# Optimization experiments

Hardware: AMD Instinct MI355X
Metric: run time of the kernel (lower is better)

Reference implementation:

```python
import jax, jax.numpy as jnp
import numpy as np

N_ATOMS = 50000
N_PAIRS = 600000
F = 128          # number_of_per_atom_features
RBF = 16         # number_of_radial_basis_functions
N_INT_RES = 3    # interaction residual blocks
N_OUT_RES = 2    # output residual blocks
N_PROPS = 2      # atomic properties (hardcoded in PhysNetModule)


def setup_inputs() -> dict:
    key = jax.random.key(0)
    ks = jax.random.split(key, 24)
    s = 1.0 / np.sqrt(F)
    inp = {
        "atomic_embedding": jax.random.normal(ks[0], (N_ATOMS, F), jnp.float32),
        "f_ij": jax.random.uniform(ks[1], (N_PAIRS, RBF), jnp.float32),
        "pair_indices": jax.random.randint(ks[2], (2, N_PAIRS), 0, N_ATOMS, jnp.int64),
        # attention_mask: Dense(RBF -> F, bias=False); zero-init in source, randomized here
        "Wg": jax.random.normal(ks[3], (RBF, F), jnp.float32) * (1.0 / np.sqrt(RBF)),
        "Wi": jax.random.normal(ks[4], (F, F), jnp.float32) * s,
        "bi": jnp.zeros((F,), jnp.float32),
        "Wj": jax.random.normal(ks[5], (F, F), jnp.float32) * s,
        "bj": jnp.zeros((F,), jnp.float32),
        "Wv": jax.random.normal(ks[6], (F, F), jnp.float32) * s,
        "bv": jnp.zeros((F,), jnp.float32),
        "gate": jnp.ones((F,), jnp.float32),
        "int_res_W1": jax.random.normal(ks[7], (N_INT_RES, F, F), jnp.float32) * s,
        "int_res_b1": jnp.zeros((N_INT_RES, F), jnp.float32),
        "int_res_W2": jax.random.normal(ks[8], (N_INT_RES, F, F), jnp.float32) * s,
        "int_res_b2": jnp.zeros((N_INT_RES, F), jnp.float32),
        "out_res_W1": jax.random.normal(ks[9], (N_OUT_RES, F, F), jnp.float32) * s,
        "out_res_b1": jnp.zeros((N_OUT_RES, F), jnp.float32),
        "out_res_W2": jax.random.normal(ks[10], (N_OUT_RES, F, F), jnp.float32) * s,
        "out_res_b2": jnp.zeros((N_OUT_RES, F), jnp.float32),
        # output head: Dense(F -> 2), zero-init in source, randomized here
        "Wo": jax.random.normal(ks[11], (F, N_PROPS), jnp.float32) * s,
        "bo": jnp.zeros((N_PROPS,), jnp.float32),
    }
    return inp


def _residual(x, W1, b1, W2, b2):
    # PhysNetResidual: x + Dense(Dense(act(x), act), linear)
    h = jax.nn.softplus(x)
    h = jax.nn.softplus(h @ W1 + b1)
    return x + h @ W2 + b2


def reference(atomic_embedding, f_ij, pair_indices,
              Wg, Wi, bi, Wj, bj, Wv, bv, gate,
              int_res_W1, int_res_b1, int_res_W2, int_res_b2,
              out_res_W1, out_res_b1, out_res_W2, out_res_b2,
              Wo, bo):
    idx_i, idx_j = pair_indices[0], pair_indices[1]

    # --- interaction module ---
    e = jax.nn.softplus(atomic_embedding)            # [N, F]
    g = f_ij @ Wg                                    # [E, F] attention mask (no bias)
    u = jax.nn.softplus(e @ Wi + bi)                 # [N, F] interaction_i
    m_j = jax.nn.softplus(e[idx_j] @ Wj + bj) * g    # [E, F] gather + gate
    u = u.at[idx_i].add(m_j)                         # scatter_add to i-atoms
    for k in range(N_INT_RES):
        u = _residual(u, int_res_W1[k], int_res_b1[k], int_res_W2[k], int_res_b2[k])
    u = jax.nn.softplus(u)
    v = gate * e + (u @ Wv + bv)                     # updated embedding [N, F]

    # --- output module ---
    x = v
    for k in range(N_OUT_RES):
        x = _residual(x, out_res_W1[k], out_res_b1[k], out_res_W2[k], out_res_b2[k])
    prediction = x @ Wo + bo                         # [N, 2]
    return prediction, v
```

## Files before the change

### kernel.cpp

```cpp
#include <hip/hip_runtime.h>
#include <math.h>

#define F 128
#define RBF 16
#define NATOMS 50000
#define NPAIRS 600000
#define NBLK 196

typedef float f32x4 __attribute__((ext_vector_type(4)));
typedef short s16x8 __attribute__((ext_vector_type(8)));

__device__ __forceinline__ float sp(float x) {
    return fmaxf(x, 0.f) + __logf(1.f + __expf(-fabsf(x)));
}
__device__ __forceinline__ short f2bf(float x) {
    unsigned u = __float_as_uint(x);
    u += 0x7FFFu + ((u >> 16) & 1u);
    return (short)(u >> 16);
}
__device__ __forceinline__ float bf2f(unsigned short u) {
    return __uint_as_float(((unsigned)u) << 16);
}

__global__ __launch_bounds__(256) void prep_w_k(
    const float* __restrict__ Wi, const float* __restrict__ Wj, const float* __restrict__ Wv,
    const float* __restrict__ iW1, const float* __restrict__ iW2,
    const float* __restrict__ oW1, const float* __restrict__ oW2,
    short* __restrict__ wpack)
{
    int o = blockIdx.x * 256 + threadIdx.x;
    if (o >= 13 * 16384) return;
    int mat = o >> 14;
    int rem = o & 16383;
    int j = rem & 7;
    int lane = (rem >> 3) & 63;
    int nt = (rem >> 9) & 7;
    int kc = rem >> 12;
    int k = kc * 32 + ((lane >> 4) << 3) + j;
    int n = nt * 16 + (lane & 15);
    const float* src;
    if (mat == 0) src = Wi;
    else if (mat == 1) src = Wj;
    else if (mat == 2) src = Wv;
    else if (mat < 6) src = iW1 + (size_t)(mat - 3) * 16384;
    else if (mat < 9) src = iW2 + (size_t)(mat - 6) * 16384;
    else if (mat < 11) src = oW1 + (size_t)(mat - 9) * 16384;
    else src = oW2 + (size_t)(mat - 11) * 16384;
    wpack[o] = f2bf(src[(size_t)k * F + n]);
}

template <int PRE>
__device__ __forceinline__ s16x8 load_a_frag(const float* __restrict__ in,
                                             int row, int nrows, int kc, int cg)
{
    s16x8 a;
    if (row < nrows) {
        const float* p = in + (size_t)row * F + kc * 32 + cg * 8;
        float4 x0 = *(const float4*)p;
        float4 x1 = *(const float4*)(p + 4);
        if (PRE) {
            x0.x = sp(x0.x); x0.y = sp(x0.y); x0.z = sp(x0.z); x0.w = sp(x0.w);
            x1.x = sp(x1.x); x1.y = sp(x1.y); x1.z = sp(x1.z); x1.w = sp(x1.w);
        }
        a[0] = f2bf(x0.x); a[1] = f2bf(x0.y); a[2] = f2bf(x0.z); a[3] = f2bf(x0.w);
        a[4] = f2bf(x1.x); a[5] = f2bf(x1.y); a[6] = f2bf(x1.z); a[7] = f2bf(x1.w);
    } else {
#pragma unroll
        for (int i = 0; i < 8; ++i) a[i] = 0;
    }
    return a;
}

template <int PRE, int POST, int DUAL>
__global__ __launch_bounds__(256) void mgemm_k(
    const float* __restrict__ in, const short* __restrict__ wpA,
    const float* __restrict__ bA, float* __restrict__ outA,
    const short* __restrict__ wpB, const float* __restrict__ bB,
    unsigned short* __restrict__ outB, int nrows)
{
    const int lane = threadIdx.x & 63;
    const int wv = threadIdx.x >> 6;
    const int grp = wv >> 1, half = wv & 1;
    const int r0 = blockIdx.x * 32 + grp * 16;
    const int cl = lane & 15, cg = lane >> 4;
    const int ntb = half * 4;

    s16x8 afr[4];
#pragma unroll
    for (int kc = 0; kc < 4; ++kc) afr[kc] = load_a_frag<PRE>(in, r0 + cl, nrows, kc, cg);

    f32x4 accA[4], accB[4];
#pragma unroll
    for (int n = 0; n < 4; ++n) {
        accA[n] = (f32x4){0.f, 0.f, 0.f, 0.f};
        accB[n] = (f32x4){0.f, 0.f, 0.f, 0.f};
    }

#pragma unroll
    for (int kc = 0; kc < 4; ++kc) {
        const s16x8* bpA = (const s16x8*)wpA + (size_t)(kc * 8 + ntb) * 64 + lane;
#pragma unroll
        for (int n = 0; n < 4; ++n) {
            s16x8 b = bpA[n * 64];
            accA[n] = __builtin_amdgcn_mfma_f32_16x16x32_bf16(afr[kc], b, accA[n], 0, 0, 0);
        }
        if (DUAL) {
            const s16x8* bpB = (const s16x8*)wpB + (size_t)(kc * 8 + ntb) * 64 + lane;
#pragma unroll
            for (int n = 0; n < 4; ++n) {
                s16x8 b = bpB[n * 64];
                accB[n] = __builtin_amdgcn_mfma_f32_16x16x32_bf16(afr[kc], b, accB[n], 0, 0, 0);
            }
        }
    }

#pragma unroll
    for (int n = 0; n < 4; ++n) {
        const int col = (ntb + n) * 16 + cl;
        const float ba = bA[col];
        const float bb = DUAL ? bB[col] : 0.f;
#pragma unroll
        for (int q = 0; q < 4; ++q) {
            const int row = r0 + cg * 4 + q;
            if (row < nrows) {
                const size_t o = (size_t)row * F + col;
                float val = accA[n][q] + ba;
                if (POST == 1) val = sp(val);
                outA[o] = val;
                if (DUAL) outB[o] = (unsigned short)f2bf(sp(accB[n][q] + bb));
            }
        }
    }
}

__device__ __forceinline__ void gemm_half(const short* __restrict__ wp, int lane, int ntb,
                                          const s16x8 afr[4], f32x4 acc[4])
{
#pragma unroll
    for (int n = 0; n < 4; ++n) acc[n] = (f32x4){0.f, 0.f, 0.f, 0.f};
#pragma unroll
    for (int kc = 0; kc < 4; ++kc) {
        const s16x8* bp = (const s16x8*)wp + (size_t)(kc * 8 + ntb) * 64 + lane;
#pragma unroll
        for (int n = 0; n < 4; ++n) {
            s16x8 b = bp[n * 64];
            acc[n] = __builtin_amdgcn_mfma_f32_16x16x32_bf16(afr[kc], b, acc[n], 0, 0, 0);
        }
    }
}

template <int FIRST>
__device__ __forceinline__ void residual_half(
    const float* __restrict__ u, f32x4 xreg[4],
    unsigned short* __restrict__ S, unsigned short* __restrict__ H,
    const short* __restrict__ wp1, const float* __restrict__ b1,
    const short* __restrict__ wp2, const float* __restrict__ b2,
    int r0, int nrows, int lane, int cl, int cg, int ntb)
{
    s16x8 afr[4];
    if (FIRST) {
#pragma unroll
        for (int kc = 0; kc < 4; ++kc) afr[kc] = load_a_frag<1>(u, r0 + cl, nrows, kc, cg);
    } else {
#pragma unroll
        for (int kc = 0; kc < 4; ++kc)
            afr[kc] = *(const s16x8*)(S + cl * 144 + kc * 32 + cg * 8);
    }
    f32x4 acc[4];
    gemm_half(wp1, lane, ntb, afr, acc);
#pragma unroll
    for (int n = 0; n < 4; ++n) {
        const int col = (ntb + n) * 16 + cl;
        const float bb = b1[col];
#pragma unroll
        for (int q = 0; q < 4; ++q)
            H[(cg * 4 + q) * 144 + col] = (unsigned short)f2bf(sp(acc[n][q] + bb));
    }
    __syncthreads();
#pragma unroll
    for (int kc = 0; kc < 4; ++kc)
        afr[kc] = *(const s16x8*)(H + cl * 144 + kc * 32 + cg * 8);
    gemm_half(wp2, lane, ntb, afr, acc);
#pragma unroll
    for (int n = 0; n < 4; ++n) {
        const int col = (ntb + n) * 16 + cl;
        const float bb = b2[col];
#pragma unroll
        for (int q = 0; q < 4; ++q) {
            float xv = xreg[n][q] + acc[n][q] + bb;
            xreg[n][q] = xv;
            S[(cg * 4 + q) * 144 + col] = (unsigned short)f2bf(sp(xv));
        }
    }
    __syncthreads();
}

__global__ __launch_bounds__(256, 4) void fused_tail_k(
    const float* __restrict__ u, const float* __restrict__ emb,
    const float* __restrict__ gate,
    const short* __restrict__ wpI1, const float* __restrict__ ib1,
    const short* __restrict__ wpI2, const float* __restrict__ ib2,
    const short* __restrict__ wpWv, const float* __restrict__ bvv,
    const short* __restrict__ wpO1, const float* __restrict__ ob1,
    const short* __restrict__ wpO2, const float* __restrict__ ob2,
    const float* __restrict__ Wo, const float* __restrict__ bo,
    float* __restrict__ vout, float* __restrict__ pred, int nrows)
{
    __shared__ unsigned short Sb[2][16 * 144];
    __shared__ unsigned short Hb[2][16 * 144];
    const int lane = threadIdx.x & 63;
    const int wv = threadIdx.x >> 6;
    const int grp = wv >> 1, half = wv & 1;
    const int r0 = blockIdx.x * 32 + grp * 16;
    const int cl = lane & 15, cg = lane >> 4;
    const int ntb = half * 4;
    unsigned short* S = Sb[grp];
    unsigned short* H = Hb[grp];

    f32x4 xreg[4];
#pragma unroll
    for (int n = 0; n < 4; ++n) {
        const int col = (ntb + n) * 16 + cl;
#pragma unroll
        for (int q = 0; q < 4; ++q) {
            const int row = r0 + cg * 4 + q;
            xreg[n][q] = (row < nrows) ? u[(size_t)row * F + col] : 0.f;
        }
    }

    residual_half<1>(u, xreg, S, H, wpI1, ib1, wpI2, ib2,
                     r0, nrows, lane, cl, cg, ntb);
    for (int k = 1; k < 3; ++k)
        residual_half<0>(u, xreg, S, H,
                         wpI1 + (size_t)k * 16384, ib1 + (size_t)k * F,
                         wpI2 + (size_t)k * 16384, ib2 + (size_t)k * F,
                         r0, nrows, lane, cl, cg, ntb);

    {
        s16x8 afr[4];
#pragma unroll
        for (int kc = 0; kc < 4; ++kc)
            afr[kc] = *(const s16x8*)(S + cl * 144 + kc * 32 + cg * 8);
        f32x4 acc[4];
        gemm_half(wpWv, lane, ntb, afr, acc);
        __syncthreads();
#pragma unroll
        for (int n = 0; n < 4; ++n) {
            const int col = (ntb + n) * 16 + cl;
            const float bb = bvv[col];
            const float gt = gate[col];
#pragma unroll
            for (int q = 0; q < 4; ++q) {
                const int row = r0 + cg * 4 + q;
                float val = acc[n][q] + bb;
                if (row < nrows) {
                    const size_t o = (size_t)row * F + col;
                    val += gt * sp(emb[o]);
                    vout[o] = val;
                }
                xreg[n][q] = val;
                S[(cg * 4 + q) * 144 + col] = (unsigned short)f2bf(sp(val));
            }
        }
        __syncthreads();
    }

    for (int k = 0; k < 2; ++k)
        residual_half<0>(u, xreg, S, H,
                         wpO1 + (size_t)k * 16384, ob1 + (size_t)k * F,
                         wpO2 + (size_t)k * 16384, ob2 + (size_t)k * F,
                         r0, nrows, lane, cl, cg, ntb);

    {
        float2 wo[4];
#pragma unroll
        for (int n = 0; n < 4; ++n)
            wo[n] = *(const float2*)(Wo + (size_t)((ntb + n) * 16 + cl) * 2);
        float* sc = (float*)S;
#pragma unroll
        for (int q = 0; q < 4; ++q) {
            float a0 = xreg[0][q] * wo[0].x + xreg[1][q] * wo[1].x
                     + xreg[2][q] * wo[2].x + xreg[3][q] * wo[3].x;
            float a1 = xreg[0][q] * wo[0].y + xreg[1][q] * wo[1].y
                     + xreg[2][q] * wo[2].y + xreg[3][q] * wo[3].y;
#pragma unroll
            for (int m = 1; m < 16; m <<= 1) {
                a0 += __shfl_xor(a0, m);
                a1 += __shfl_xor(a1, m);
            }
            if (cl == 0) {
                sc[half * 32 + (cg * 4 + q) * 2 + 0] = a0;
                sc[half * 32 + (cg * 4 + q) * 2 + 1] = a1;
            }
        }
        __syncthreads();
        if (half == 0 && lane < 16) {
            const int row = r0 + lane;
            if (row < nrows) {
                pred[(size_t)row * 2 + 0] = sc[lane * 2 + 0] + sc[32 + lane * 2 + 0] + bo[0];
                pred[(size_t)row * 2 + 1] = sc[lane * 2 + 1] + sc[32 + lane * 2 + 1] + bo[1];
            }
        }
    }
}

__global__ void zero_k(int* __restrict__ p, int n)
{
    int i = blockIdx.x * blockDim.x + threadIdx.x;
    if (i < n) p[i] = 0;
}

__global__ void hist_k(const int* __restrict__ idx_i, int* __restrict__ counts)
{
    int p = blockIdx.x * blockDim.x + threadIdx.x;
    if (p < NPAIRS) atomicAdd(&counts[idx_i[p]], 1);
}

__global__ __launch_bounds__(256) void scan1_k(
    const int* __restrict__ counts, int* __restrict__ bsum)
{
    __shared__ int red[256];
    const int t = threadIdx.x;
    const int i = blockIdx.x * 256 + t;
    red[t] = (i < NATOMS) ? counts[i] : 0;
    __syncthreads();
#pragma unroll
    for (int s = 128; s > 0; s >>= 1) {
        if (t < s) red[t] += red[t + s];
        __syncthreads();
    }
    if (t == 0) bsum[blockIdx.x] = red[0];
}

__global__ __launch_bounds__(256) void scan2_k(
    const int* __restrict__ bsum, int* __restrict__ bbase, int* __restrict__ offsets)
{
    __shared__ int sh[256];
    const int t = threadIdx.x;
    const int v = (t < NBLK) ? bsum[t] : 0;
    sh[t] = v;
    __syncthreads();
#pragma unroll
    for (int s = 1; s < 256; s <<= 1) {
        int add = (t >= s) ? sh[t - s] : 0;
        __syncthreads();
        sh[t] += add;
        __syncthreads();
    }
    if (t < NBLK) bbase[t] = sh[t] - v;
    if (t == 0) offsets[NATOMS] = NPAIRS;
}

__global__ __launch_bounds__(256) void scan3_k(
    const int* __restrict__ counts, const int* __restrict__ bbase,
    int* __restrict__ offsets, int* __restrict__ cursor)
{
    __shared__ int sh[256];
    const int t = threadIdx.x;
    const int i = blockIdx.x * 256 + t;
    const int v = (i < NATOMS) ? counts[i] : 0;
    sh[t] = v;
    __syncthreads();
#pragma unroll
    for (int s = 1; s < 256; s <<= 1) {
        int add = (t >= s) ? sh[t - s] : 0;
        __syncthreads();
        sh[t] += add;
        __syncthreads();
    }
    if (i < NATOMS) {
        const int off = bbase[blockIdx.x] + sh[t] - v;
        offsets[i] = off;
        cursor[i] = off;
    }
}

__global__ void scatter_k(const int* __restrict__ idx_i, const int* __restrict__ idx_j,
                          int* __restrict__ cursor, int* __restrict__ plist,
                          int* __restrict__ jlist)
{
    int p = blockIdx.x * blockDim.x + threadIdx.x;
    if (p < NPAIRS) {
        int pos = atomicAdd(&cursor[idx_i[p]], 1);
        plist[pos] = p;
        jlist[pos] = idx_j[p];
    }
}

__device__ __forceinline__ void gpair(const float* __restrict__ fp,
                                      const float* wg0, const float* wg1,
                                      float& g0, float& g1)
{
    float4 A = ((const float4*)fp)[0], B = ((const float4*)fp)[1];
    float4 C = ((const float4*)fp)[2], D = ((const float4*)fp)[3];
    g0 = A.x*wg0[0] + A.y*wg0[1] + A.z*wg0[2] + A.w*wg0[3]
       + B.x*wg0[4] + B.y*wg0[5] + B.z*wg0[6] + B.w*wg0[7]
       + C.x*wg0[8] + C.y*wg0[9] + C.z*wg0[10] + C.w*wg0[11]
       + D.x*wg0[12] + D.y*wg0[13] + D.z*wg0[14] + D.w*wg0[15];
    g1 = A.x*wg1[0] + A.y*wg1[1] + A.z*wg1[2] + A.w*wg1[3]
       + B.x*wg1[4] + B.y*wg1[5] + B.z*wg1[6] + B.w*wg1[7]
       + C.x*wg1[8] + C.y*wg1[9] + C.z*wg1[10] + C.w*wg1[11]
       + D.x*wg1[12] + D.y*wg1[13] + D.z*wg1[14] + D.w*wg1[15];
}

__global__ __launch_bounds__(256) void gather_k(
    const unsigned short* __restrict__ mj, const float* __restrict__ fij,
    const int* __restrict__ jlist, const int* __restrict__ plist,
    const int* __restrict__ offsets, const float* __restrict__ Wg,
    float* __restrict__ u)
{
    const int lane = threadIdx.x & 63;
    const int atom = blockIdx.x * 4 + (threadIdx.x >> 6);
    const int f0 = lane * 2;

    float wg0[16], wg1[16];
#pragma unroll
    for (int r = 0; r < 16; ++r) {
        float2 w = *(const float2*)(Wg + r * F + f0);
        wg0[r] = w.x; wg1[r] = w.y;
    }

    const int k0 = offsets[atom], k1 = offsets[atom + 1];
    float acc0 = 0.f, acc1 = 0.f;

    for (int k = k0; k < k1; k += 8) {
        int jv[8], pv[8];
#pragma unroll
        for (int t = 0; t < 8; ++t) {
            const int kk = (k + t < k1) ? (k + t) : (k1 - 1);
            jv[t] = jlist[kk];
            pv[t] = plist[kk];
        }
        unsigned m[8];
        const float* fp[8];
#pragma unroll
        for (int t = 0; t < 8; ++t) {
            const int js = __builtin_amdgcn_readfirstlane(jv[t]);
            const int ps = __builtin_amdgcn_readfirstlane(pv[t]);
            m[t] = *(const unsigned*)(mj + (size_t)js * F + f0);
            fp[t] = fij + (size_t)ps * RBF;
        }
#pragma unroll
        for (int t = 0; t < 8; ++t) {
            float g0, g1;
            gpair(fp[t], wg0, wg1, g0, g1);
            if (k + t >= k1) { g0 = 0.f; g1 = 0.f; }
            acc0 += bf2f((unsigned short)(m[t] & 0xFFFF)) * g0;
            acc1 += bf2f((unsigned short)(m[t] >> 16))    * g1;
        }
    }

    float2* up = (float2*)(u + (size_t)atom * F + f0);
    float2 old = *up;
    old.x += acc0; old.y += acc1;
    *up = old;
}

extern "C" void kernel_launch(void* const* d_in, const int* in_sizes, int n_in,
                              void* d_out, int out_size, void* d_ws, size_t ws_size,
                              hipStream_t stream)
{
    const float* emb   = (const float*)d_in[0];
    const float* fij   = (const float*)d_in[1];
    const int*   pidx  = (const int*)d_in[2];
    const float* Wg    = (const float*)d_in[3];
    const float* Wi    = (const float*)d_in[4];
    const float* bi    = (const float*)d_in[5];
    const float* Wj    = (const float*)d_in[6];
    const float* bj    = (const float*)d_in[7];
    const float* Wv    = (const float*)d_in[8];
    const float* bv    = (const float*)d_in[9];
    const float* gate  = (const float*)d_in[10];
    const float* iW1   = (const float*)d_in[11];
    const float* ib1   = (const float*)d_in[12];
    const float* iW2   = (const float*)d_in[13];
    const float* ib2   = (const float*)d_in[14];
    const float* oW1   = (const float*)d_in[15];
    const float* ob1   = (const float*)d_in[16];
    const float* oW2   = (const float*)d_in[17];
    const float* ob2   = (const float*)d_in[18];
    const float* Wo    = (const float*)d_in[19];
    const float* bo    = (const float*)d_in[20];

    const int* idx_i = pidx;
    const int* idx_j = pidx + NPAIRS;

    float* outp = (float*)d_out;
    float* pred = outp;
    float* v    = outp + (size_t)NATOMS * 2;

    const size_t NF = (size_t)NATOMS * F;
    float* u = (float*)d_ws;
    unsigned short* mj = (unsigned short*)(u + NF);
    short* wpack = (short*)(mj + NF);
    int* counts   = (int*)(wpack + 13 * 16384);
    int* offsets  = counts + NATOMS;
    int* cursor   = offsets + NATOMS + 1;
    int* plist    = cursor + NATOMS;
    int* jlist    = plist + NPAIRS;
    int* bsum     = jlist + NPAIRS;
    int* bbase    = bsum + NBLK;

    const short* wpWi = wpack;
    const short* wpWj = wpack + 1 * 16384;
    const short* wpWv = wpack + 2 * 16384;
    const short* wpI1 = wpack + 3 * 16384;
    const short* wpI2 = wpack + 6 * 16384;
    const short* wpO1 = wpack + 9 * 16384;
    const short* wpO2 = wpack + 11 * 16384;

    prep_w_k<<<(13 * 16384 + 255) / 256, 256, 0, stream>>>(Wi, Wj, Wv, iW1, iW2, oW1, oW2, wpack);
    zero_k<<<(NATOMS + 255) / 256, 256, 0, stream>>>(counts, NATOMS);
    hist_k<<<(NPAIRS + 255) / 256, 256, 0, stream>>>(idx_i, counts);
    scan1_k<<<NBLK, 256, 0, stream>>>(counts, bsum);
    scan2_k<<<1, 256, 0, stream>>>(bsum, bbase, offsets);
    scan3_k<<<NBLK, 256, 0, stream>>>(counts, bbase, offsets, cursor);
    scatter_k<<<(NPAIRS + 255) / 256, 256, 0, stream>>>(idx_i, idx_j, cursor, plist, jlist);

    mgemm_k<1, 1, 1><<<(NATOMS + 31) / 32, 256, 0, stream>>>(
        emb, wpWi, bi, u, wpWj, bj, mj, NATOMS);

    gather_k<<<(NATOMS + 3) / 4, 256, 0, stream>>>(
        mj, fij, jlist, plist, offsets, Wg, u);

    fused_tail_k<<<(NATOMS + 31) / 32, 256, 0, stream>>>(
        u, emb, gate,
        wpI1, ib1, wpI2, ib2,
        wpWv, bv,
        wpO1, ob1, wpO2, ob2,
        Wo, bo, v, pred, NATOMS);
}
```

Before: 267.6 us.

## Split fused tail across four waves per 16-row tile with swizzled LDS

After: 280.3 us. 4.8% more time.

```diff
diff --git a/kernel.cpp b/kernel.cpp
--- a/kernel.cpp
+++ b/kernel.cpp
@@ -13,13 +13,16 @@
 __device__ __forceinline__ float sp(float x) {
     return fmaxf(x, 0.f) + __logf(1.f + __expf(-fabsf(x)));
 }
-__device__ __forceinline__ short f2bf(float x) {
+__device__ __forceinline__ unsigned short f2bf(float x) {
     unsigned u = __float_as_uint(x);
     u += 0x7FFFu + ((u >> 16) & 1u);
-    return (short)(u >> 16);
+    return (unsigned short)(u >> 16);
 }
 __device__ __forceinline__ float bf2f(unsigned short u) {
     return __uint_as_float(((unsigned)u) << 16);
+}
+__device__ __forceinline__ int lds_idx(int row, int col) {
+    return (row * 144 + col) ^ ((row & 7) << 3);
 }
 
 __global__ __launch_bounds__(256) void prep_w_k(
@@ -46,7 +49,7 @@
     else if (mat < 9) src = iW2 + (size_t)(mat - 6) * 16384;
     else if (mat < 11) src = oW1 + (size_t)(mat - 9) * 16384;
     else src = oW2 + (size_t)(mat - 11) * 16384;
-    wpack[o] = f2bf(src[(size_t)k * F + n]);
+    wpack[o] = (short)f2bf(src[(size_t)k * F + n]);
 }
 
 template <int PRE>
@@ -127,22 +130,22 @@
                 float val = accA[n][q] + ba;
                 if (POST == 1) val = sp(val);
                 outA[o] = val;
-                if (DUAL) outB[o] = (unsigned short)f2bf(sp(accB[n][q] + bb));
+                if (DUAL) outB[o] = f2bf(sp(accB[n][q] + bb));
             }
         }
     }
 }
 
-__device__ __forceinline__ void gemm_half(const short* __restrict__ wp, int lane, int ntb,
-                                          const s16x8 afr[4], f32x4 acc[4])
-{
-#pragma unroll
-    for (int n = 0; n < 4; ++n) acc[n] = (f32x4){0.f, 0.f, 0.f, 0.f};
+__device__ __forceinline__ void gemm_q(const short* __restrict__ wp, int lane, int ntb,
+                                       const s16x8 afr[4], f32x4 acc[2])
+{
+#pragma unroll
+    for (int n = 0; n < 2; ++n) acc[n] = (f32x4){0.f, 0.f, 0.f, 0.f};
 #pragma unroll
     for (int kc = 0; kc < 4; ++kc) {
         const s16x8* bp = (const s16x8*)wp + (size_t)(kc * 8 + ntb) * 64 + lane;
 #pragma unroll
-        for (int n = 0; n < 4; ++n) {
+        for (int n = 0; n < 2; ++n) {
             s16x8 b = bp[n * 64];
             acc[n] = __builtin_amdgcn_mfma_f32_16x16x32_bf16(afr[kc], b, acc[n], 0, 0, 0);
         }
@@ -150,8 +153,8 @@
 }
 
 template <int FIRST>
-__device__ __forceinline__ void residual_half(
-    const float* __restrict__ u, f32x4 xreg[4],
+__device__ __forceinline__ void residual_q(
+    const float* __restrict__ u, f32x4 xreg[2],
     unsigned short* __restrict__ S, unsigned short* __restrict__ H,
     const short* __restrict__ wp1, const float* __restrict__ b1,
     const short* __restrict__ wp2, const float* __restrict__ b2,
@@ -164,38 +167,38 @@
     } else {
 #pragma unroll
         for (int kc = 0; kc < 4; ++kc)
-            afr[kc] = *(const s16x8*)(S + cl * 144 + kc * 32 + cg * 8);
-    }
-    f32x4 acc[4];
-    gemm_half(wp1, lane, ntb, afr, acc);
-#pragma unroll
-    for (int n = 0; n < 4; ++n) {
+            afr[kc] = *(const s16x8*)(S + lds_idx(cl, kc * 32 + cg * 8));
+    }
+    f32x4 acc[2];
+    gemm_q(wp1, lane, ntb, afr, acc);
+#pragma unroll
+    for (int n = 0; n < 2; ++n) {
         const int col = (ntb + n) * 16 + cl;
         const float bb = b1[col];
 #pragma unroll
         for (int q = 0; q < 4; ++q)
-            H[(cg * 4 + q) * 144 + col] = (unsigned short)f2bf(sp(acc[n][q] + bb));
+            H[lds_idx(cg * 4 + q, col)] = f2bf(sp(acc[n][q] + bb));
     }
     __syncthreads();
 #pragma unroll
     for (int kc = 0; kc < 4; ++kc)
-        afr[kc] = *(const s16x8*)(H + cl * 144 + kc * 32 + cg * 8);
-    gemm_half(wp2, lane, ntb, afr, acc);
-#pragma unroll
-    for (int n = 0; n < 4; ++n) {
+        afr[kc] = *(const s16x8*)(H + lds_idx(cl, kc * 32 + cg * 8));
+    gemm_q(wp2, lane, ntb, afr, acc);
+#pragma unroll
+    for (int n = 0; n < 2; ++n) {
         const int col = (ntb + n) * 16 + cl;
         const float bb = b2[col];
 #pragma unroll
         for (int q = 0; q < 4; ++q) {
             float xv = xreg[n][q] + acc[n][q] + bb;
             xreg[n][q] = xv;
-            S[(cg * 4 + q) * 144 + col] = (unsigned short)f2bf(sp(xv));
+            S[lds_idx(cg * 4 + q, col)] = f2bf(sp(xv));
         }
     }
     __syncthreads();
 }
 
-__global__ __launch_bounds__(256, 4) void fused_tail_k(
+__global__ __launch_bounds__(256, 6) void fused_tail_k(
     const float* __restrict__ u, const float* __restrict__ emb,
     const float* __restrict__ gate,
     const short* __restrict__ wpI1, const float* __restrict__ ib1,
@@ -206,20 +209,17 @@
     const float* __restrict__ Wo, const float* __restrict__ bo,
     float* __restrict__ vout, float* __restrict__ pred, int nrows)
 {
-    __shared__ unsigned short Sb[2][16 * 144];
-    __shared__ unsigned short Hb[2][16 * 144];
+    __shared__ unsigned short S[16 * 144];
+    __shared__ unsigned short H[16 * 144];
     const int lane = threadIdx.x & 63;
     const int wv = threadIdx.x >> 6;
-    const int grp = wv >> 1, half = wv & 1;
-    const int r0 = blockIdx.x * 32 + grp * 16;
+    const int r0 = blockIdx.x * 16;
     const int cl = lane & 15, cg = lane >> 4;
-    const int ntb = half * 4;
-    unsigned short* S = Sb[grp];
-    unsigned short* H = Hb[grp];
-
-    f32x4 xreg[4];
-#pragma unroll
-    for (int n = 0; n < 4; ++n) {
+    const int ntb = wv * 2;
+
+    f32x4 xreg[2];
+#pragma unroll
+    for (int n = 0; n < 2; ++n) {
         const int col = (ntb + n) * 16 + cl;
 #pragma unroll
         for (int q = 0; q < 4; ++q) {
@@ -228,24 +228,24 @@
         }
     }
 
-    residual_half<1>(u, xreg, S, H, wpI1, ib1, wpI2, ib2,
-                     r0, nrows, lane, cl, cg, ntb);
+    residual_q<1>(u, xreg, S, H, wpI1, ib1, wpI2, ib2,
+                  r0, nrows, lane, cl, cg, ntb);
     for (int k = 1; k < 3; ++k)
-        residual_half<0>(u, xreg, S, H,
-                         wpI1 + (size_t)k * 16384, ib1 + (size_t)k * F,
-                         wpI2 + (size_t)k * 16384, ib2 + (size_t)k * F,
-                         r0, nrows, lane, cl, cg, ntb);
+        residual_q<0>(u, xreg, S, H,
+                      wpI1 + (size_t)k * 16384, ib1 + (size_t)k * F,
+                      wpI2 + (size_t)k * 16384, ib2 + (size_t)k * F,
+                      r0, nrows, lane, cl, cg, ntb);
 
     {
         s16x8 afr[4];
 #pragma unroll
         for (int kc = 0; kc < 4; ++kc)
-            afr[kc] = *(const s16x8*)(S + cl * 144 + kc * 32 + cg * 8);
-        f32x4 acc[4];
-        gemm_half(wpWv, lane, ntb, afr, acc);
-        __syncthreads();
-#pragma unroll
-        for (int n = 0; n < 4; ++n) {
+            afr[kc] = *(const s16x8*)(S + lds_idx(cl, kc * 32 + cg * 8));
+        f32x4 acc[2];
+        gemm_q(wpWv, lane, ntb, afr, acc);
+        __syncthreads();
+#pragma unroll
+        for (int n = 0; n < 2; ++n) {
             const int col = (ntb + n) * 16 + cl;
             const float bb = bvv[col];
             const float gt = gate[col];
@@ -259,55 +259,49 @@
                     vout[o] = val;
                 }
                 xreg[n][q] = val;
-                S[(cg * 4 + q) * 144 + col] = (unsigned short)f2bf(sp(val));
+                S[lds_idx(cg * 4 + q, col)] = f2bf(sp(val));
             }
         }
         __syncthreads();
     }
 
     for (int k = 0; k < 2; ++k)
-        residual_half<0>(u, xreg, S, H,
-                         wpO1 + (size_t)k * 16384, ob1 + (size_t)k * F,
-                         wpO2 + (size_t)k * 16384, ob2 + (size_t)k * F,
-                         r0, nrows, lane, cl, cg, ntb);
+        residual_q<0>(u, xreg, S, H,
+                      wpO1 + (size_t)k * 16384, ob1 + (size_t)k * F,
+                      wpO2 + (size_t)k * 16384, ob2 + (size_t)k * F,
+                      r0, nrows, lane, cl, cg, ntb);
 
     {
-        float2 wo[4];
-#pragma unroll
-        for (int n = 0; n < 4; ++n)
+        float2 wo[2];
+#pragma unroll
+        for (int n = 0; n < 2; ++n)
             wo[n] = *(const float2*)(Wo + (size_t)((ntb + n) * 16 + cl) * 2);
         float* sc = (float*)S;
 #pragma unroll
         for (int q = 0; q < 4; ++q) {
-            float a0 = xreg[0][q] * wo[0].x + xreg[1][q] * wo[1].x
-                     + xreg[2][q] * wo[2].x + xreg[3][q] * wo[3].x;
-            float a1 = xreg[0][q] * wo[0].y + xreg[1][q] * wo[1].y
-                     + xreg[2][q] * wo[2].y + xreg[3][q] * wo[3].y;
+            float a0 = xreg[0][q] * wo[0].x + xreg[1][q] * wo[1].x;
+            float a1 = xreg[0][q] * wo[0].y + xreg[1][q] * wo[1].y;
 #pragma unroll
             for (int m = 1; m < 16; m <<= 1) {
                 a0 += __shfl_xor(a0, m);
                 a1 += __shfl_xor(a1, m);
             }
             if (cl == 0) {
-                sc[half * 32 + (cg * 4 + q) * 2 + 0] = a0;
-                sc[half * 32 + (cg * 4 + q) * 2 + 1] = a1;
+                sc[wv * 32 + (cg * 4 + q) * 2 + 0] = a0;
+                sc[wv * 32 + (cg * 4 + q) * 2 + 1] = a1;
             }
         }
         __syncthreads();
-        if (half == 0 && lane < 16) {
+        if (wv == 0 && lane < 16) {
             const int row = r0 + lane;
             if (row < nrows) {
-                pred[(size_t)row * 2 + 0] = sc[lane * 2 + 0] + sc[32 + lane * 2 + 0] + bo[0];
-                pred[(size_t)row * 2 + 1] = sc[lane * 2 + 1] + sc[32 + lane * 2 + 1] + bo[1];
+                pred[(size_t)row * 2 + 0] = sc[lane * 2 + 0] + sc[32 + lane * 2 + 0]
+                                          + sc[64 + lane * 2 + 0] + sc[96 + lane * 2 + 0] + bo[0];
+                pred[(size_t)row * 2 + 1] = sc[lane * 2 + 1] + sc[32 + lane * 2 + 1]
+                                          + sc[64 + lane * 2 + 1] + sc[96 + lane * 2 + 1] + bo[1];
             }
         }
     }
-}
-
-__global__ void zero_k(int* __restrict__ p, int n)
-{
-    int i = blockIdx.x * blockDim.x + threadIdx.x;
-    if (i < n) p[i] = 0;
 }
 
 __global__ void hist_k(const int* __restrict__ idx_i, int* __restrict__ counts)
@@ -510,7 +504,7 @@
     const short* wpO2 = wpack + 11 * 16384;
 
     prep_w_k<<<(13 * 16384 + 255) / 256, 256, 0, stream>>>(Wi, Wj, Wv, iW1, iW2, oW1, oW2, wpack);
-    zero_k<<<(NATOMS + 255) / 256, 256, 0, stream>>>(counts, NATOMS);
+    hipMemsetAsync(counts, 0, NATOMS * sizeof(int), stream);
     hist_k<<<(NPAIRS + 255) / 256, 256, 0, stream>>>(idx_i, counts);
     scan1_k<<<NBLK, 256, 0, stream>>>(counts, bsum);
     scan2_k<<<1, 256, 0, stream>>>(bsum, bbase, offsets);
@@ -523,7 +517,7 @@
     gather_k<<<(NATOMS + 3) / 4, 256, 0, stream>>>(
         mj, fij, jlist, plist, offsets, Wg, u);
 
-    fused_tail_k<<<(NATOMS + 31) / 32, 256, 0, stream>>>(
+    fused_tail_k<<<(NATOMS + 15) / 16, 256, 0, stream>>>(
         u, emb, gate,
         wpI1, ib1, wpI2, ib2,
         wpWv, bv,
```

## Fuse gather-scatter aggregation into the residual tail kernel via shared memory

Applied to the files above, without the earlier changes.

New measurement: 306.9 us. +14.7%, slower.

```diff
diff --git a/kernel.cpp b/kernel.cpp
--- a/kernel.cpp
+++ b/kernel.cpp
@@ -13,10 +13,10 @@
 __device__ __forceinline__ float sp(float x) {
     return fmaxf(x, 0.f) + __logf(1.f + __expf(-fabsf(x)));
 }
-__device__ __forceinline__ short f2bf(float x) {
+__device__ __forceinline__ unsigned short f2bf(float x) {
     unsigned u = __float_as_uint(x);
     u += 0x7FFFu + ((u >> 16) & 1u);
-    return (short)(u >> 16);
+    return (unsigned short)(u >> 16);
 }
 __device__ __forceinline__ float bf2f(unsigned short u) {
     return __uint_as_float(((unsigned)u) << 16);
@@ -46,7 +46,7 @@
     else if (mat < 9) src = iW2 + (size_t)(mat - 6) * 16384;
     else if (mat < 11) src = oW1 + (size_t)(mat - 9) * 16384;
     else src = oW2 + (size_t)(mat - 11) * 16384;
-    wpack[o] = f2bf(src[(size_t)k * F + n]);
+    wpack[o] = (short)f2bf(src[(size_t)k * F + n]);
 }
 
 template <int PRE>
@@ -127,7 +127,7 @@
                 float val = accA[n][q] + ba;
                 if (POST == 1) val = sp(val);
                 outA[o] = val;
-                if (DUAL) outB[o] = (unsigned short)f2bf(sp(accB[n][q] + bb));
+                if (DUAL) outB[o] = f2bf(sp(accB[n][q] + bb));
             }
         }
     }
@@ -151,7 +151,7 @@
 
 template <int FIRST>
 __device__ __forceinline__ void residual_half(
-    const float* __restrict__ u, f32x4 xreg[4],
+    const float* __restrict__ u, const float* __restrict__ sug, f32x4 xreg[4],
     unsigned short* __restrict__ S, unsigned short* __restrict__ H,
     const short* __restrict__ wp1, const float* __restrict__ b1,
     const short* __restrict__ wp2, const float* __restrict__ b2,
@@ -159,8 +159,27 @@
 {
     s16x8 afr[4];
     if (FIRST) {
-#pragma unroll
-        for (int kc = 0; kc < 4; ++kc) afr[kc] = load_a_frag<1>(u, r0 + cl, nrows, kc, cg);
+        const int row = r0 + cl;
+#pragma unroll
+        for (int kc = 0; kc < 4; ++kc) {
+            s16x8 a;
+            if (row < nrows) {
+                const float* p = u + (size_t)row * F + kc * 32 + cg * 8;
+                float4 x0 = *(const float4*)p;
+                float4 x1 = *(const float4*)(p + 4);
+                const float* sq = sug + cl * 132 + kc * 32 + cg * 8;
+                f32x4 s0 = *(const f32x4*)sq;
+                f32x4 s1 = *(const f32x4*)(sq + 4);
+                a[0] = f2bf(sp(x0.x + s0.x)); a[1] = f2bf(sp(x0.y + s0.y));
+                a[2] = f2bf(sp(x0.z + s0.z)); a[3] = f2bf(sp(x0.w + s0.w));
+                a[4] = f2bf(sp(x1.x + s1.x)); a[5] = f2bf(sp(x1.y + s1.y));
+                a[6] = f2bf(sp(x1.z + s1.z)); a[7] = f2bf(sp(x1.w + s1.w));
+            } else {
+#pragma unroll
+                for (int i = 0; i < 8; ++i) a[i] = 0;
+            }
+            afr[kc] = a;
+        }
     } else {
 #pragma unroll
         for (int kc = 0; kc < 4; ++kc)
@@ -174,7 +193,7 @@
         const float bb = b1[col];
 #pragma unroll
         for (int q = 0; q < 4; ++q)
-            H[(cg * 4 + q) * 144 + col] = (unsigned short)f2bf(sp(acc[n][q] + bb));
+            H[(cg * 4 + q) * 144 + col] = f2bf(sp(acc[n][q] + bb));
     }
     __syncthreads();
 #pragma unroll
@@ -189,202 +208,10 @@
         for (int q = 0; q < 4; ++q) {
             float xv = xreg[n][q] + acc[n][q] + bb;
             xreg[n][q] = xv;
-            S[(cg * 4 + q) * 144 + col] = (unsigned short)f2bf(sp(xv));
+            S[(cg * 4 + q) * 144 + col] = f2bf(sp(xv));
         }
     }
     __syncthreads();
-}
-
-__global__ __launch_bounds__(256, 4) void fused_tail_k(
-    const float* __restrict__ u, const float* __restrict__ emb,
-    const float* __restrict__ gate,
-    const short* __restrict__ wpI1, const float* __restrict__ ib1,
-    const short* __restrict__ wpI2, const float* __restrict__ ib2,
-    const short* __restrict__ wpWv, const float* __restrict__ bvv,
-    const short* __restrict__ wpO1, const float* __restrict__ ob1,
-    const short* __restrict__ wpO2, const float* __restrict__ ob2,
-    const float* __restrict__ Wo, const float* __restrict__ bo,
-    float* __restrict__ vout, float* __restrict__ pred, int nrows)
-{
-    __shared__ unsigned short Sb[2][16 * 144];
-    __shared__ unsigned short Hb[2][16 * 144];
-    const int lane = threadIdx.x & 63;
-    const int wv = threadIdx.x >> 6;
-    const int grp = wv >> 1, half = wv & 1;
-    const int r0 = blockIdx.x * 32 + grp * 16;
-    const int cl = lane & 15, cg = lane >> 4;
-    const int ntb = half * 4;
-    unsigned short* S = Sb[grp];
-    unsigned short* H = Hb[grp];
-
-    f32x4 xreg[4];
-#pragma unroll
-    for (int n = 0; n < 4; ++n) {
-        const int col = (ntb + n) * 16 + cl;
-#pragma unroll
-        for (int q = 0; q < 4; ++q) {
-            const int row = r0 + cg * 4 + q;
-            xreg[n][q] = (row < nrows) ? u[(size_t)row * F + col] : 0.f;
-        }
-    }
-
-    residual_half<1>(u, xreg, S, H, wpI1, ib1, wpI2, ib2,
-                     r0, nrows, lane, cl, cg, ntb);
-    for (int k = 1; k < 3; ++k)
-        residual_half<0>(u, xreg, S, H,
-                         wpI1 + (size_t)k * 16384, ib1 + (size_t)k * F,
-                         wpI2 + (size_t)k * 16384, ib2 + (size_t)k * F,
-                         r0, nrows, lane, cl, cg, ntb);
-
-    {
-        s16x8 afr[4];
-#pragma unroll
-        for (int kc = 0; kc < 4; ++kc)
-            afr[kc] = *(const s16x8*)(S + cl * 144 + kc * 32 + cg * 8);
-        f32x4 acc[4];
-        gemm_half(wpWv, lane, ntb, afr, acc);
-        __syncthreads();
-#pragma unroll
-        for (int n = 0; n < 4; ++n) {
-            const int col = (ntb + n) * 16 + cl;
-            const float bb = bvv[col];
-            const float gt = gate[col];
-#pragma unroll
-            for (int q = 0; q < 4; ++q) {
-                const int row = r0 + cg * 4 + q;
-                float val = acc[n][q] + bb;
-                if (row < nrows) {
-                    const size_t o = (size_t)row * F + col;
-                    val += gt * sp(emb[o]);
-                    vout[o] = val;
-                }
-                xreg[n][q] = val;
-                S[(cg * 4 + q) * 144 + col] = (unsigned short)f2bf(sp(val));
-            }
-        }
-        __syncthreads();
-    }
-
-    for (int k = 0; k < 2; ++k)
-        residual_half<0>(u, xreg, S, H,
-                         wpO1 + (size_t)k * 16384, ob1 + (size_t)k * F,
-                         wpO2 + (size_t)k * 16384, ob2 + (size_t)k * F,
-                         r0, nrows, lane, cl, cg, ntb);
-
-    {
-        float2 wo[4];
-#pragma unroll
-        for (int n = 0; n < 4; ++n)
-            wo[n] = *(const float2*)(Wo + (size_t)((ntb + n) * 16 + cl) * 2);
-        float* sc = (float*)S;
-#pragma unroll
-        for (int q = 0; q < 4; ++q) {
-            float a0 = xreg[0][q] * wo[0].x + xreg[1][q] * wo[1].x
-                     + xreg[2][q] * wo[2].x + xreg[3][q] * wo[3].x;
-            float a1 = xreg[0][q] * wo[0].y + xreg[1][q] * wo[1].y
-                     + xreg[2][q] * wo[2].y + xreg[3][q] * wo[3].y;
-#pragma unroll
-            for (int m = 1; m < 16; m <<= 1) {
-                a0 += __shfl_xor(a0, m);
-                a1 += __shfl_xor(a1, m);
-            }
-            if (cl == 0) {
-                sc[half * 32 + (cg * 4 + q) * 2 + 0] = a0;
-                sc[half * 32 + (cg * 4 + q) * 2 + 1] = a1;
-            }
-        }
-        __syncthreads();
-        if (half == 0 && lane < 16) {
-            const int row = r0 + lane;
-            if (row < nrows) {
-                pred[(size_t)row * 2 + 0] = sc[lane * 2 + 0] + sc[32 + lane * 2 + 0] + bo[0];
-                pred[(size_t)row * 2 + 1] = sc[lane * 2 + 1] + sc[32 + lane * 2 + 1] + bo[1];
-            }
-        }
-    }
-}
-
-__global__ void zero_k(int* __restrict__ p, int n)
-{
-    int i = blockIdx.x * blockDim.x + threadIdx.x;
-    if (i < n) p[i] = 0;
-}
-
-__global__ void hist_k(const int* __restrict__ idx_i, int* __restrict__ counts)
-{
-    int p = blockIdx.x * blockDim.x + threadIdx.x;
-    if (p < NPAIRS) atomicAdd(&counts[idx_i[p]], 1);
-}
-
-__global__ __launch_bounds__(256) void scan1_k(
-    const int* __restrict__ counts, int* __restrict__ bsum)
-{
-    __shared__ int red[256];
-    const int t = threadIdx.x;
-    const int i = blockIdx.x * 256 + t;
-    red[t] = (i < NATOMS) ? counts[i] : 0;
-    __syncthreads();
-#pragma unroll
-    for (int s = 128; s > 0; s >>= 1) {
-        if (t < s) red[t] += red[t + s];
-        __syncthreads();
-    }
-    if (t == 0) bsum[blockIdx.x] = red[0];
-}
-
-__global__ __launch_bounds__(256) void scan2_k(
-    const int* __restrict__ bsum, int* __restrict__ bbase, int* __restrict__ offsets)
-{
-    __shared__ int sh[256];
-    const int t = threadIdx.x;
-    const int v = (t < NBLK) ? bsum[t] : 0;
-    sh[t] = v;
-    __syncthreads();
-#pragma unroll
-    for (int s = 1; s < 256; s <<= 1) {
-        int add = (t >= s) ? sh[t - s] : 0;
-        __syncthreads();
-        sh[t] += add;
-        __syncthreads();
-    }
-    if (t < NBLK) bbase[t] = sh[t] - v;
-    if (t == 0) offsets[NATOMS] = NPAIRS;
-}
-
-__global__ __launch_bounds__(256) void scan3_k(
-    const int* __restrict__ counts, const int* __restrict__ bbase,
-    int* __restrict__ offsets, int* __restrict__ cursor)
-{
-    __shared__ int sh[256];
-    const int t = threadIdx.x;
-    const int i = blockIdx.x * 256 + t;
-    const int v = (i < NATOMS) ? counts[i] : 0;
-    sh[t] = v;
-    __syncthreads();
-#pragma unroll
-    for (int s = 1; s < 256; s <<= 1) {
-        int add = (t >= s) ? sh[t - s] : 0;
-        __syncthreads();
-        sh[t] += add;
-        __syncthreads();
-    }
-    if (i < NATOMS) {
-        const int off = bbase[blockIdx.x] + sh[t] - v;
-        offsets[i] = off;
-        cursor[i] = off;
-    }
-}
-
-__global__ void scatter_k(const int* __restrict__ idx_i, const int* __restrict__ idx_j,
-                          int* __restrict__ cursor, int* __restrict__ plist,
-                          int* __restrict__ jlist)
-{
-    int p = blockIdx.x * blockDim.x + threadIdx.x;
-    if (p < NPAIRS) {
-        int pos = atomicAdd(&cursor[idx_i[p]], 1);
-        plist[pos] = p;
-        jlist[pos] = idx_j[p];
-    }
 }
 
 __device__ __forceinline__ void gpair(const float* __restrict__ fp,
@@ -403,57 +230,245 @@
        + D.x*wg1[12] + D.y*wg1[13] + D.z*wg1[14] + D.w*wg1[15];
 }
 
-__global__ __launch_bounds__(256) void gather_k(
-    const unsigned short* __restrict__ mj, const float* __restrict__ fij,
+__global__ __launch_bounds__(256, 4) void gtail_k(
+    const float* __restrict__ u, const unsigned short* __restrict__ mj,
+    const float* __restrict__ fij,
     const int* __restrict__ jlist, const int* __restrict__ plist,
     const int* __restrict__ offsets, const float* __restrict__ Wg,
-    float* __restrict__ u)
-{
+    const float* __restrict__ emb, const float* __restrict__ gate,
+    const short* __restrict__ wpI1, const float* __restrict__ ib1,
+    const short* __restrict__ wpI2, const float* __restrict__ ib2,
+    const short* __restrict__ wpWv, const float* __restrict__ bvv,
+    const short* __restrict__ wpO1, const float* __restrict__ ob1,
+    const short* __restrict__ wpO2, const float* __restrict__ ob2,
+    const float* __restrict__ Wo, const float* __restrict__ bo,
+    float* __restrict__ vout, float* __restrict__ pred, int nrows)
+{
+    __shared__ float su[32 * 132];
+    __shared__ unsigned short Sb[2][16 * 144];
+    __shared__ unsigned short Hb[2][16 * 144];
     const int lane = threadIdx.x & 63;
-    const int atom = blockIdx.x * 4 + (threadIdx.x >> 6);
-    const int f0 = lane * 2;
-
-    float wg0[16], wg1[16];
-#pragma unroll
-    for (int r = 0; r < 16; ++r) {
-        float2 w = *(const float2*)(Wg + r * F + f0);
-        wg0[r] = w.x; wg1[r] = w.y;
-    }
-
-    const int k0 = offsets[atom], k1 = offsets[atom + 1];
-    float acc0 = 0.f, acc1 = 0.f;
-
-    for (int k = k0; k < k1; k += 8) {
-        int jv[8], pv[8];
-#pragma unroll
+    const int wv = threadIdx.x >> 6;
+    const int b0 = blockIdx.x * 32;
+
+    {
+        const int f0 = lane * 2;
+        float wg0[16], wg1[16];
+#pragma unroll
+        for (int r = 0; r < 16; ++r) {
+            float2 w = *(const float2*)(Wg + r * F + f0);
+            wg0[r] = w.x; wg1[r] = w.y;
+        }
         for (int t = 0; t < 8; ++t) {
-            const int kk = (k + t < k1) ? (k + t) : (k1 - 1);
-            jv[t] = jlist[kk];
-            pv[t] = plist[kk];
-        }
-        unsigned m[8];
-        const float* fp[8];
-#pragma unroll
-        for (int t = 0; t < 8; ++t) {
-            const int js = __builtin_amdgcn_readfirstlane(jv[t]);
-            const int ps = __builtin_amdgcn_readfirstlane(pv[t]);
-            m[t] = *(const unsigned*)(mj + (size_t)js * F + f0);
-            fp[t] = fij + (size_t)ps * RBF;
-        }
-#pragma unroll
-        for (int t = 0; t < 8; ++t) {
-            float g0, g1;
-            gpair(fp[t], wg0, wg1, g0, g1);
-            if (k + t >= k1) { g0 = 0.f; g1 = 0.f; }
-            acc0 += bf2f((unsigned short)(m[t] & 0xFFFF)) * g0;
-            acc1 += bf2f((unsigned short)(m[t] >> 16))    * g1;
-        }
-    }
-
-    float2* up = (float2*)(u + (size_t)atom * F + f0);
-    float2 old = *up;
-    old.x += acc0; old.y += acc1;
-    *up = old;
+            const int lrow = wv * 8 + t;
+            const int atom = b0 + lrow;
+            float acc0 = 0.f, acc1 = 0.f;
+            if (atom < nrows) {
+                const int k0 = offsets[atom], k1 = offsets[atom + 1];
+                for (int k = k0; k < k1; k += 8) {
+                    int jv[8], pv[8];
+#pragma unroll
+                    for (int s = 0; s < 8; ++s) {
+                        const int kk = (k + s < k1) ? (k + s) : (k1 - 1);
+                        jv[s] = jlist[kk];
+                        pv[s] = plist[kk];
+                    }
+                    unsigned m[8];
+                    const float* fp[8];
+#pragma unroll
+                    for (int s = 0; s < 8; ++s) {
+                        const int js = __builtin_amdgcn_readfirstlane(jv[s]);
+                        const int ps = __builtin_amdgcn_readfirstlane(pv[s]);
+                        m[s] = *(const unsigned*)(mj + (size_t)js * F + f0);
+                        fp[s] = fij + (size_t)ps * RBF;
+                    }
+#pragma unroll
+                    for (int s = 0; s < 8; ++s) {
+                        float g0, g1;
+                        gpair(fp[s], wg0, wg1, g0, g1);
+                        if (k + s >= k1) { g0 = 0.f; g1 = 0.f; }
+                        acc0 += bf2f((unsigned short)(m[s] & 0xFFFF)) * g0;
+                        acc1 += bf2f((unsigned short)(m[s] >> 16))    * g1;
+                    }
+                }
+            }
+            su[lrow * 132 + f0]     = acc0;
+            su[lrow * 132 + f0 + 1] = acc1;
+        }
+    }
+    __syncthreads();
+
+    const int grp = wv >> 1, half = wv & 1;
+    const int r0 = b0 + grp * 16;
+    const int cl = lane & 15, cg = lane >> 4;
+    const int ntb = half * 4;
+    unsigned short* S = Sb[grp];
+    unsigned short* H = Hb[grp];
+    const float* sug = su + (size_t)(grp * 16) * 132;
+
+    f32x4 xreg[4];
+#pragma unroll
+    for (int n = 0; n < 4; ++n) {
+        const int col = (ntb + n) * 16 + cl;
+#pragma unroll
+        for (int q = 0; q < 4; ++q) {
+            const int row = r0 + cg * 4 + q;
+            float base = (row < nrows) ? u[(size_t)row * F + col] : 0.f;
+            xreg[n][q] = base + sug[(cg * 4 + q) * 132 + col];
+        }
+    }
+
+    residual_half<1>(u, sug, xreg, S, H, wpI1, ib1, wpI2, ib2,
+                     r0, nrows, lane, cl, cg, ntb);
+    for (int k = 1; k < 3; ++k)
+        residual_half<0>(u, sug, xreg, S, H,
+                         wpI1 + (size_t)k * 16384, ib1 + (size_t)k * F,
+                         wpI2 + (size_t)k * 16384, ib2 + (size_t)k * F,
+                         r0, nrows, lane, cl, cg, ntb);
+
+    {
+        s16x8 afr[4];
+#pragma unroll
+        for (int kc = 0; kc < 4; ++kc)
+            afr[kc] = *(const s16x8*)(S + cl * 144 + kc * 32 + cg * 8);
+        f32x4 acc[4];
+        gemm_half(wpWv, lane, ntb, afr, acc);
+        __syncthreads();
+#pragma unroll
+        for (int n = 0; n < 4; ++n) {
+            const int col = (ntb + n) * 16 + cl;
+            const float bb = bvv[col];
+            const float gt = gate[col];
+#pragma unroll
+            for (int q = 0; q < 4; ++q) {
+                const int row = r0 + cg * 4 + q;
+                float val = acc[n][q] + bb;
+                if (row < nrows) {
+                    const size_t o = (size_t)row * F + col;
+                    val += gt * sp(emb[o]);
+                    vout[o] = val;
+                }
+                xreg[n][q] = val;
+                S[(cg * 4 + q) * 144 + col] = f2bf(sp(val));
+            }
+        }
+        __syncthreads();
+    }
+
+    for (int k = 0; k < 2; ++k)
+        residual_half<0>(u, sug, xreg, S, H,
+                         wpO1 + (size_t)k * 16384, ob1 + (size_t)k * F,
+                         wpO2 + (size_t)k * 16384, ob2 + (size_t)k * F,
+                         r0, nrows, lane, cl, cg, ntb);
+
+    {
+        float2 wo[4];
+#pragma unroll
+        for (int n = 0; n < 4; ++n)
+            wo[n] = *(const float2*)(Wo + (size_t)((ntb + n) * 16 + cl) * 2);
+        float* sc = (float*)S;
+#pragma unroll
+        for (int q = 0; q < 4; ++q) {
+            float a0 = xreg[0][q] * wo[0].x + xreg[1][q] * wo[1].x
+                     + xreg[2][q] * wo[2].x + xreg[3][q] * wo[3].x;
+            float a1 = xreg[0][q] * wo[0].y + xreg[1][q] * wo[1].y
+                     + xreg[2][q] * wo[2].y + xreg[3][q] * wo[3].y;
+#pragma unroll
+            for (int m = 1; m < 16; m <<= 1) {
+                a0 += __shfl_xor(a0, m);
+                a1 += __shfl_xor(a1, m);
+            }
+            if (cl == 0) {
+                sc[half * 32 + (cg * 4 + q) * 2 + 0] = a0;
+                sc[half * 32 + (cg * 4 + q) * 2 + 1] = a1;
+            }
+        }
+        __syncthreads();
+        if (half == 0 && lane < 16) {
+            const int row = r0 + lane;
+            if (row < nrows) {
+                pred[(size_t)row * 2 + 0] = sc[lane * 2 + 0] + sc[32 + lane * 2 + 0] + bo[0];
+                pred[(size_t)row * 2 + 1] = sc[lane * 2 + 1] + sc[32 + lane * 2 + 1] + bo[1];
+            }
+        }
+    }
+}
+
+__global__ void hist_k(const int* __restrict__ idx_i, int* __restrict__ counts)
+{
+    int p = blockIdx.x * blockDim.x + threadIdx.x;
+    if (p < NPAIRS) atomicAdd(&counts[idx_i[p]], 1);
+}
+
+__global__ __launch_bounds__(256) void scan1_k(
+    const int* __restrict__ counts, int* __restrict__ bsum)
+{
+    __shared__ int red[256];
+    const int t = threadIdx.x;
+    const int i = blockIdx.x * 256 + t;
+    red[t] = (i < NATOMS) ? counts[i] : 0;
+    __syncthreads();
+#pragma unroll
+    for (int s = 128; s > 0; s >>= 1) {
+        if (t < s) red[t] += red[t + s];
+        __syncthreads();
+    }
+    if (t == 0) bsum[blockIdx.x] = red[0];
+}
+
+__global__ __launch_bounds__(256) void scan2_k(
+    const int* __restrict__ bsum, int* __restrict__ bbase, int* __restrict__ offsets)
+{
+    __shared__ int sh[256];
+    const int t = threadIdx.x;
+    const int v = (t < NBLK) ? bsum[t] : 0;
+    sh[t] = v;
+    __syncthreads();
+#pragma unroll
+    for (int s = 1; s < 256; s <<= 1) {
+        int add = (t >= s) ? sh[t - s] : 0;
+        __syncthreads();
+        sh[t] += add;
+        __syncthreads();
+    }
+    if (t < NBLK) bbase[t] = sh[t] - v;
+    if (t == 0) offsets[NATOMS] = NPAIRS;
+}
+
+__global__ __launch_bounds__(256) void scan3_k(
+    const int* __restrict__ counts, const int* __restrict__ bbase,
+    int* __restrict__ offsets, int* __restrict__ cursor)
+{
+    __shared__ int sh[256];
+    const int t = threadIdx.x;
+    const int i = blockIdx.x * 256 + t;
+    const int v = (i < NATOMS) ? counts[i] : 0;
+    sh[t] = v;
+    __syncthreads();
+#pragma unroll
+    for (int s = 1; s < 256; s <<= 1) {
+        int add = (t >= s) ? sh[t - s] : 0;
+        __syncthreads();
+        sh[t] += add;
+        __syncthreads();
+    }
+    if (i < NATOMS) {
+        const int off = bbase[blockIdx.x] + sh[t] - v;
+        offsets[i] = off;
+        cursor[i] = off;
+    }
+}
+
+__global__ void scatter_k(const int* __restrict__ idx_i, const int* __restrict__ idx_j,
+                          int* __restrict__ cursor, int* __restrict__ plist,
+                          int* __restrict__ jlist)
+{
+    int p = blockIdx.x * blockDim.x + threadIdx.x;
+    if (p < NPAIRS) {
+        int pos = atomicAdd(&cursor[idx_i[p]], 1);
+        plist[pos] = p;
+        jlist[pos] = idx_j[p];
+    }
 }
 
 extern "C" void kernel_launch(void* const* d_in, const int* in_sizes, int n_in,
@@ -510,7 +525,7 @@
     const short* wpO2 = wpack + 11 * 16384;
 
     prep_w_k<<<(13 * 16384 + 255) / 256, 256, 0, stream>>>(Wi, Wj, Wv, iW1, iW2, oW1, oW2, wpack);
-    zero_k<<<(NATOMS + 255) / 256, 256, 0, stream>>>(counts, NATOMS);
+    hipMemsetAsync(counts, 0, NATOMS * sizeof(int), stream);
     hist_k<<<(NPAIRS + 255) / 256, 256, 0, stream>>>(idx_i, counts);
     scan1_k<<<NBLK, 256, 0, stream>>>(counts, bsum);
     scan2_k<<<1, 256, 0, stream>>>(bsum, bbase, offsets);
@@ -520,11 +535,8 @@
     mgemm_k<1, 1, 1><<<(NATOMS + 31) / 32, 256, 0, stream>>>(
         emb, wpWi, bi, u, wpWj, bj, mj, NATOMS);
 
-    gather_k<<<(NATOMS + 3) / 4, 256, 0, stream>>>(
-        mj, fij, jlist, plist, offsets, Wg, u);
-
-    fused_tail_k<<<(NATOMS + 31) / 32, 256, 0, stream>>>(
-        u, emb, gate,
+    gtail_k<<<(NATOMS + 31) / 32, 256, 0, stream>>>(
+        u, mj, fij, jlist, plist, offsets, Wg, emb, gate,
         wpI1, ib1, wpI2, ib2,
         wpWv, bv,
         wpO1, ob1, wpO2, ob2,
```
